# Optimization experiments

Measured on AMD Instinct MI355X. Metric: run time of the kernel, lower is better.

## Reference

```python
import jax, jax.numpy as jnp
import numpy as np

S, P, C = 64, 2048, 32   # num_scenes, num_pixels, scene_channels
A, D, E = 2048, 128, 64  # agent_size, dynamics_features, embed_dim


def setup_inputs() -> dict:
    key = jax.random.key(0)
    ks = jax.random.split(key, 9)
    inv = lambda n: 1.0 / np.sqrt(n)
    return {
        "global_scene": jax.random.normal(ks[0], (S, P, C), jnp.float32),
        "scene_idx": jax.random.randint(ks[1], (A,), 0, S),
        "dynamic_encoding": jax.random.normal(ks[2], (A, D), jnp.float32),
        "W_sn": jax.random.uniform(ks[3], (C, E), jnp.float32, -inv(C), inv(C)),
        "b_sn": jax.random.uniform(ks[4], (E,), jnp.float32, -inv(C), inv(C)),
        "W_df": jax.random.uniform(ks[5], (D, E), jnp.float32, -inv(D), inv(D)),
        "b_df": jax.random.uniform(ks[6], (E,), jnp.float32, -inv(D), inv(D)),
        "w_fc": jax.random.uniform(ks[7], (E,), jnp.float32, -inv(E), inv(E)),
        "b_fc": jax.random.uniform(ks[8], (1,), jnp.float32, -inv(E), inv(E)),
    }


def reference(global_scene, scene_idx, dynamic_encoding, W_sn, b_sn, W_df, b_df, w_fc, b_fc):
    # att1: [S, P, E]; att2: [A, E]
    att1 = jnp.einsum('spc,ce->spe', global_scene, W_sn) + b_sn
    att2 = dynamic_encoding @ W_df + b_df
    # gather scenes per agent, fuse add + relu: [A, P, E]
    add_fusion = jax.nn.relu(att1[scene_idx] + att2[:, None, :])
    # linear to scalar score per pixel, softmax over pixels (dim=1)
    logits = jnp.einsum('ape,e->ap', add_fusion, w_fc) + b_fc[0]  # [A, P]
    alpha = jax.nn.softmax(logits, axis=1)[:, :, None]            # [A, P, 1]
    # alpha-weighted pooling of gathered scene features -> [A, C]
    return jnp.sum(alpha * global_scene[scene_idx], axis=1)
```

## Files before the change

### kernel.cpp

```cpp
#include <hip/hip_runtime.h>
#include <hip/hip_bf16.h>

#define S_ 64
#define P_ 2048
#define C_ 32
#define A_ 2048
#define D_ 128
#define E_ 64

#define LPX   128
#define NLCH  (P_ / LPX)

__global__ __launch_bounds__(256) void att2s_kernel(
    const float* __restrict__ de, const float* __restrict__ Wdf,
    const float* __restrict__ bdf, const int* __restrict__ sidx,
    float* __restrict__ att2, int* __restrict__ counts,
    int* __restrict__ lists, float* __restrict__ Z) {
  __shared__ float4 Wl[128 * 16];
  __shared__ float4 bl[16];
  __shared__ float  dl[16 * 128];
  const int tid = threadIdx.x;

  if (blockIdx.x == 0 && tid < A_ / 4)
    ((float4*)Z)[tid] = make_float4(0.f, 0.f, 0.f, 0.f);

  if (tid < 16) {
    const int a = blockIdx.x * 16 + tid;
    const int s = sidx[a];
    const int pos = atomicAdd(&counts[s], 1);
    lists[s * A_ + pos] = a;
  }

  const float4* W4 = (const float4*)Wdf;
#pragma unroll
  for (int i = 0; i < 8; ++i) Wl[tid + i * 256] = W4[tid + i * 256];
  if (tid < 16) bl[tid] = ((const float4*)bdf)[tid];
  const long base = (long)blockIdx.x * (16 * 128);
#pragma unroll
  for (int i = 0; i < 8; ++i) dl[tid + i * 256] = de[base + tid + i * 256];
  __syncthreads();

  const int r = tid >> 4, e4 = tid & 15;
  float4 acc = bl[e4];
#pragma unroll 4
  for (int d = 0; d < 128; ++d) {
    const float  g = dl[r * 128 + d];
    const float4 w = Wl[d * 16 + e4];
    acc.x = fmaf(g, w.x, acc.x);
    acc.y = fmaf(g, w.y, acc.y);
    acc.z = fmaf(g, w.z, acc.z);
    acc.w = fmaf(g, w.w, acc.w);
  }
  ((float4*)att2)[((long)blockIdx.x * 16 + r) * 16 + e4] = acc;
}

__global__ __launch_bounds__(256) void fused_kernel(
    const float* __restrict__ gs, const float* __restrict__ Wsn,
    const float* __restrict__ bsn, const float* __restrict__ wfc,
    const float* __restrict__ att2, const int* __restrict__ counts,
    const int* __restrict__ lists, float* __restrict__ partial,
    float* __restrict__ Z) {
  const int s   = blockIdx.x >> 4;
  const int ch  = blockIdx.x & (NLCH - 1);
  const int p0  = ch * LPX;
  const int tid = threadIdx.x;
  const int px  = tid >> 1;
  const int eh  = tid & 1;

  __shared__ float  gsl[LPX][36];
  __shared__ float  ubuf[32 * 132];
  __shared__ float4 a2l[32][16];
  __shared__ int    aidl[32];

  float4* Wl4 = (float4*)ubuf;
  float (*alpha_l)[132] = (float(*)[132])ubuf;

  const float4* W4 = (const float4*)Wsn;
  Wl4[tid]       = W4[tid];
  Wl4[tid + 256] = W4[tid + 256];

  const float4* g4 = (const float4*)(gs + ((long)s * P_ + p0) * C_);
#pragma unroll
  for (int k = 0; k < 4; ++k) {
    const int f = tid + k * 256;
    const float4 v = g4[f];
    const int pp = f >> 3, c0 = (f & 7) * 4;
    gsl[pp][c0]     = v.x;
    gsl[pp][c0 + 1] = v.y;
    gsl[pp][c0 + 2] = v.z;
    gsl[pp][c0 + 3] = v.w;
  }

  const float4* wf4 = (const float4*)wfc;
  const float4* b4  = (const float4*)bsn;
  float4 wf[8], a1[8];
#pragma unroll
  for (int q = 0; q < 8; ++q) { wf[q] = wf4[eh * 8 + q]; a1[q] = b4[eh * 8 + q]; }
  __syncthreads();

#pragma unroll
  for (int c = 0; c < 32; ++c) {
    const float g = gsl[px][c];
#pragma unroll
    for (int q = 0; q < 8; ++q) {
      const float4 w = Wl4[c * 16 + eh * 8 + q];
      a1[q].x = fmaf(g, w.x, a1[q].x);
      a1[q].y = fmaf(g, w.y, a1[q].y);
      a1[q].z = fmaf(g, w.z, a1[q].z);
      a1[q].w = fmaf(g, w.w, a1[q].w);
    }
  }

  const int j2 = tid >> 3;
  const int c4 = tid & 7;
  const int n_s = counts[s];

  for (int g0 = 0; g0 < n_s; g0 += 32) {
    const int m = min(32, n_s - g0);
    __syncthreads();
#pragma unroll
    for (int k = 0; k < 2; ++k) {
      const int idx = tid + k * 256;
      const int j = idx >> 4, e4 = idx & 15;
      if (j < m) {
        const int aj = lists[s * A_ + g0 + j];
        a2l[j][e4] = ((const float4*)att2)[aj * 16 + e4];
        if (e4 == 0) aidl[j] = aj;
      }
    }
    __syncthreads();

    for (int j = 0; j < m; ++j) {
      float c0 = 0.f, c1 = 0.f, c2 = 0.f, c3 = 0.f;
#pragma unroll
      for (int q = 0; q < 8; ++q) {
        const float4 t = a2l[j][eh * 8 + q];
        const float4 w = wf[q];
        const float4 av = a1[q];
        c0 = fmaf(fmaxf(av.x + t.x, 0.f), w.x, c0);
        c1 = fmaf(fmaxf(av.y + t.y, 0.f), w.y, c1);
        c2 = fmaf(fmaxf(av.z + t.z, 0.f), w.z, c2);
        c3 = fmaf(fmaxf(av.w + t.w, 0.f), w.w, c3);
      }
      float r = (c0 + c1) + (c2 + c3);
      r += __shfl_xor(r, 1);
      if (eh == 0) alpha_l[j][px] = __expf(r);
    }
    __syncthreads();

    if (j2 < m) {
      const int a = aidl[j2];
      float4 a0 = make_float4(0.f, 0.f, 0.f, 0.f);
      float4 a1p = make_float4(0.f, 0.f, 0.f, 0.f);
      float4 a2p = make_float4(0.f, 0.f, 0.f, 0.f);
      float4 a3p = make_float4(0.f, 0.f, 0.f, 0.f);
      float  zs = 0.f;
#pragma unroll 4
      for (int p4 = 0; p4 < LPX / 4; ++p4) {
        const float w0 = alpha_l[j2][p4 * 4 + 0];
        const float w1 = alpha_l[j2][p4 * 4 + 1];
        const float w2 = alpha_l[j2][p4 * 4 + 2];
        const float w3 = alpha_l[j2][p4 * 4 + 3];
        const float4 v0 = *(const float4*)&gsl[p4 * 4 + 0][c4 * 4];
        const float4 v1 = *(const float4*)&gsl[p4 * 4 + 1][c4 * 4];
        const float4 v2 = *(const float4*)&gsl[p4 * 4 + 2][c4 * 4];
        const float4 v3 = *(const float4*)&gsl[p4 * 4 + 3][c4 * 4];
        zs += (w0 + w1) + (w2 + w3);
        a0.x = fmaf(w0, v0.x, a0.x); a0.y = fmaf(w0, v0.y, a0.y);
        a0.z = fmaf(w0, v0.z, a0.z); a0.w = fmaf(w0, v0.w, a0.w);
        a1p.x = fmaf(w1, v1.x, a1p.x); a1p.y = fmaf(w1, v1.y, a1p.y);
        a1p.z = fmaf(w1, v1.z, a1p.z); a1p.w = fmaf(w1, v1.w, a1p.w);
        a2p.x = fmaf(w2, v2.x, a2p.x); a2p.y = fmaf(w2, v2.y, a2p.y);
        a2p.z = fmaf(w2, v2.z, a2p.z); a2p.w = fmaf(w2, v2.w, a2p.w);
        a3p.x = fmaf(w3, v3.x, a3p.x); a3p.y = fmaf(w3, v3.y, a3p.y);
        a3p.z = fmaf(w3, v3.z, a3p.z); a3p.w = fmaf(w3, v3.w, a3p.w);
      }
      const float4 acc = make_float4((a0.x + a1p.x) + (a2p.x + a3p.x),
                                     (a0.y + a1p.y) + (a2p.y + a3p.y),
                                     (a0.z + a1p.z) + (a2p.z + a3p.z),
                                     (a0.w + a1p.w) + (a2p.w + a3p.w));
      *(float4*)(partial + (long)ch * (A_ * C_) + (long)a * C_ + c4 * 4) = acc;
      if (c4 == 0) atomicAdd(&Z[a], zs);
    }
  }
}

__global__ __launch_bounds__(256) void norm_kernel(
    const float* __restrict__ partial, const float* __restrict__ Z,
    float* __restrict__ out) {
  const int i = blockIdx.x * 256 + threadIdx.x;
  float sum = 0.f;
#pragma unroll
  for (int ch = 0; ch < NLCH; ++ch) sum += partial[(long)ch * (A_ * C_) + i];
  out[i] = sum / Z[i >> 5];
}

extern "C" void kernel_launch(void* const* d_in, const int* in_sizes, int n_in,
                              void* d_out, int out_size, void* d_ws, size_t ws_size,
                              hipStream_t stream) {
  const float* gs   = (const float*)d_in[0];
  const int*   sidx = (const int*)  d_in[1];
  const float* de   = (const float*)d_in[2];
  const float* Wsn  = (const float*)d_in[3];
  const float* bsn  = (const float*)d_in[4];
  const float* Wdf  = (const float*)d_in[5];
  const float* bdf  = (const float*)d_in[6];
  const float* wfc  = (const float*)d_in[7];
  float* out = (float*)d_out;

  float* att2    = (float*)d_ws;
  float* Z       = att2 + (long)A_ * E_;
  int*   counts  = (int*)(Z + A_);
  int*   lists   = counts + 64;
  float* partial = (float*)(lists + (long)S_ * A_);

  hipMemsetAsync(counts, 0, 64 * sizeof(int), stream);
  att2s_kernel<<<A_ / 16,   256, 0, stream>>>(de, Wdf, bdf, sidx, att2,
                                              counts, lists, Z);
  fused_kernel<<<S_ * NLCH, 256, 0, stream>>>(gs, Wsn, bsn, wfc, att2,
                                              counts, lists, partial, Z);
  norm_kernel <<<(A_ * C_) / 256, 256, 0, stream>>>(partial, Z, out);
}
```

Baseline: 141.7 us.

## Fuse normalization into main kernel via last-block reduction and drop memset

Folds the final partial-sum normalization into the fused kernel: each chunk block bumps a per-scene counter, and the last block for a scene reduces the 16 partials and divides by Z. Scene list building moves to a single block doing a deterministic scan, which removes the memset launch and the global atomics. The agent group size drops from 32 to 16, and pooling now uses float2 per thread so all 256 threads stay busy. In exchange, block 0 of the prep kernel runs a serial 2048-iteration scan per scene, the tail reduction runs on only 64 blocks, and the added group iterations bring more barriers.

Result: slower. 288.9 us (+103.9%).

```diff
diff --git a/kernel.cpp b/kernel.cpp
--- a/kernel.cpp
+++ b/kernel.cpp
@@ -1,5 +1,4 @@
 #include <hip/hip_runtime.h>
-#include <hip/hip_bf16.h>
 
 #define S_ 64
 #define P_ 2048
@@ -8,27 +7,32 @@
 #define D_ 128
 #define E_ 64
 
-#define LPX   128
-#define NLCH  (P_ / LPX)
-
-__global__ __launch_bounds__(256) void att2s_kernel(
+#define LPX  128
+#define NLCH (P_ / LPX)
+#define GRP  16
+
+__global__ __launch_bounds__(256) void prep_kernel(
     const float* __restrict__ de, const float* __restrict__ Wdf,
     const float* __restrict__ bdf, const int* __restrict__ sidx,
     float* __restrict__ att2, int* __restrict__ counts,
-    int* __restrict__ lists, float* __restrict__ Z) {
+    int* __restrict__ lists, float* __restrict__ Z,
+    int* __restrict__ scene_done) {
   __shared__ float4 Wl[128 * 16];
   __shared__ float4 bl[16];
   __shared__ float  dl[16 * 128];
+  __shared__ int    sl[A_];
   const int tid = threadIdx.x;
 
-  if (blockIdx.x == 0 && tid < A_ / 4)
-    ((float4*)Z)[tid] = make_float4(0.f, 0.f, 0.f, 0.f);
-
-  if (tid < 16) {
-    const int a = blockIdx.x * 16 + tid;
-    const int s = sidx[a];
-    const int pos = atomicAdd(&counts[s], 1);
-    lists[s * A_ + pos] = a;
+  if (blockIdx.x == 0) {
+    for (int i = tid; i < A_; i += 256) { Z[i] = 0.f; sl[i] = sidx[i]; }
+    if (tid < S_) scene_done[tid] = 0;
+    __syncthreads();
+    if (tid < S_) {
+      int cnt = 0;
+      for (int a = 0; a < A_; ++a)
+        if (sl[a] == tid) lists[tid * A_ + cnt++] = a;
+      counts[tid] = cnt;
+    }
   }
 
   const float4* W4 = (const float4*)Wdf;
@@ -59,7 +63,8 @@
     const float* __restrict__ bsn, const float* __restrict__ wfc,
     const float* __restrict__ att2, const int* __restrict__ counts,
     const int* __restrict__ lists, float* __restrict__ partial,
-    float* __restrict__ Z) {
+    float* __restrict__ Z, int* __restrict__ scene_done,
+    float* __restrict__ out) {
   const int s   = blockIdx.x >> 4;
   const int ch  = blockIdx.x & (NLCH - 1);
   const int p0  = ch * LPX;
@@ -68,9 +73,10 @@
   const int eh  = tid & 1;
 
   __shared__ float  gsl[LPX][36];
-  __shared__ float  ubuf[32 * 132];
-  __shared__ float4 a2l[32][16];
-  __shared__ int    aidl[32];
+  __shared__ float  ubuf[GRP * 132];
+  __shared__ float4 a2l[GRP][16];
+  __shared__ int    aidl[GRP];
+  __shared__ int    lastFlag;
 
   float4* Wl4 = (float4*)ubuf;
   float (*alpha_l)[132] = (float(*)[132])ubuf;
@@ -111,17 +117,15 @@
     }
   }
 
-  const int j2 = tid >> 3;
-  const int c4 = tid & 7;
+  const int j2 = tid >> 4;
+  const int cp = tid & 15;
   const int n_s = counts[s];
 
-  for (int g0 = 0; g0 < n_s; g0 += 32) {
-    const int m = min(32, n_s - g0);
-    __syncthreads();
-#pragma unroll
-    for (int k = 0; k < 2; ++k) {
-      const int idx = tid + k * 256;
-      const int j = idx >> 4, e4 = idx & 15;
+  for (int g0 = 0; g0 < n_s; g0 += GRP) {
+    const int m = min(GRP, n_s - g0);
+    __syncthreads();
+    {
+      const int j = tid >> 4, e4 = tid & 15;
       if (j < m) {
         const int aj = lists[s * A_ + g0 + j];
         a2l[j][e4] = ((const float4*)att2)[aj * 16 + e4];
@@ -150,49 +154,51 @@
 
     if (j2 < m) {
       const int a = aidl[j2];
-      float4 a0 = make_float4(0.f, 0.f, 0.f, 0.f);
-      float4 a1p = make_float4(0.f, 0.f, 0.f, 0.f);
-      float4 a2p = make_float4(0.f, 0.f, 0.f, 0.f);
-      float4 a3p = make_float4(0.f, 0.f, 0.f, 0.f);
+      float2 s0 = make_float2(0.f, 0.f), s1 = make_float2(0.f, 0.f);
+      float2 s2 = make_float2(0.f, 0.f), s3 = make_float2(0.f, 0.f);
       float  zs = 0.f;
 #pragma unroll 4
-      for (int p4 = 0; p4 < LPX / 4; ++p4) {
-        const float w0 = alpha_l[j2][p4 * 4 + 0];
-        const float w1 = alpha_l[j2][p4 * 4 + 1];
-        const float w2 = alpha_l[j2][p4 * 4 + 2];
-        const float w3 = alpha_l[j2][p4 * 4 + 3];
-        const float4 v0 = *(const float4*)&gsl[p4 * 4 + 0][c4 * 4];
-        const float4 v1 = *(const float4*)&gsl[p4 * 4 + 1][c4 * 4];
-        const float4 v2 = *(const float4*)&gsl[p4 * 4 + 2][c4 * 4];
-        const float4 v3 = *(const float4*)&gsl[p4 * 4 + 3][c4 * 4];
+      for (int p = 0; p < LPX; p += 4) {
+        const float w0 = alpha_l[j2][p + 0];
+        const float w1 = alpha_l[j2][p + 1];
+        const float w2 = alpha_l[j2][p + 2];
+        const float w3 = alpha_l[j2][p + 3];
+        const float2 v0 = *(const float2*)&gsl[p + 0][cp * 2];
+        const float2 v1 = *(const float2*)&gsl[p + 1][cp * 2];
+        const float2 v2 = *(const float2*)&gsl[p + 2][cp * 2];
+        const float2 v3 = *(const float2*)&gsl[p + 3][cp * 2];
         zs += (w0 + w1) + (w2 + w3);
-        a0.x = fmaf(w0, v0.x, a0.x); a0.y = fmaf(w0, v0.y, a0.y);
-        a0.z = fmaf(w0, v0.z, a0.z); a0.w = fmaf(w0, v0.w, a0.w);
-        a1p.x = fmaf(w1, v1.x, a1p.x); a1p.y = fmaf(w1, v1.y, a1p.y);
-        a1p.z = fmaf(w1, v1.z, a1p.z); a1p.w = fmaf(w1, v1.w, a1p.w);
-        a2p.x = fmaf(w2, v2.x, a2p.x); a2p.y = fmaf(w2, v2.y, a2p.y);
-        a2p.z = fmaf(w2, v2.z, a2p.z); a2p.w = fmaf(w2, v2.w, a2p.w);
-        a3p.x = fmaf(w3, v3.x, a3p.x); a3p.y = fmaf(w3, v3.y, a3p.y);
-        a3p.z = fmaf(w3, v3.z, a3p.z); a3p.w = fmaf(w3, v3.w, a3p.w);
+        s0.x = fmaf(w0, v0.x, s0.x); s0.y = fmaf(w0, v0.y, s0.y);
+        s1.x = fmaf(w1, v1.x, s1.x); s1.y = fmaf(w1, v1.y, s1.y);
+        s2.x = fmaf(w2, v2.x, s2.x); s2.y = fmaf(w2, v2.y, s2.y);
+        s3.x = fmaf(w3, v3.x, s3.x); s3.y = fmaf(w3, v3.y, s3.y);
       }
-      const float4 acc = make_float4((a0.x + a1p.x) + (a2p.x + a3p.x),
-                                     (a0.y + a1p.y) + (a2p.y + a3p.y),
-                                     (a0.z + a1p.z) + (a2p.z + a3p.z),
-                                     (a0.w + a1p.w) + (a2p.w + a3p.w));
-      *(float4*)(partial + (long)ch * (A_ * C_) + (long)a * C_ + c4 * 4) = acc;
-      if (c4 == 0) atomicAdd(&Z[a], zs);
-    }
-  }
-}
-
-__global__ __launch_bounds__(256) void norm_kernel(
-    const float* __restrict__ partial, const float* __restrict__ Z,
-    float* __restrict__ out) {
-  const int i = blockIdx.x * 256 + threadIdx.x;
-  float sum = 0.f;
-#pragma unroll
-  for (int ch = 0; ch < NLCH; ++ch) sum += partial[(long)ch * (A_ * C_) + i];
-  out[i] = sum / Z[i >> 5];
+      const float2 acc = make_float2((s0.x + s1.x) + (s2.x + s3.x),
+                                     (s0.y + s1.y) + (s2.y + s3.y));
+      *(float2*)(partial + (long)ch * (A_ * C_) + (long)a * C_ + cp * 2) = acc;
+      if (cp == 0) atomicAdd(&Z[a], zs);
+    }
+  }
+
+  __syncthreads();
+  if (tid == 0) {
+    __threadfence();
+    lastFlag = (atomicAdd(&scene_done[s], 1) == NLCH - 1);
+  }
+  __syncthreads();
+  if (lastFlag) {
+    __threadfence();
+    for (int i = tid; i < n_s * C_; i += 256) {
+      const int j = i >> 5;
+      const int c = i & 31;
+      const int a = lists[s * A_ + j];
+      float sum = 0.f;
+#pragma unroll
+      for (int cc = 0; cc < NLCH; ++cc)
+        sum += partial[(long)cc * (A_ * C_) + (long)a * C_ + c];
+      out[(long)a * C_ + c] = sum / Z[a];
+    }
+  }
 }
 
 extern "C" void kernel_launch(void* const* d_in, const int* in_sizes, int n_in,
@@ -208,16 +214,16 @@
   const float* wfc  = (const float*)d_in[7];
   float* out = (float*)d_out;
 
-  float* att2    = (float*)d_ws;
-  float* Z       = att2 + (long)A_ * E_;
-  int*   counts  = (int*)(Z + A_);
-  int*   lists   = counts + 64;
-  float* partial = (float*)(lists + (long)S_ * A_);
-
-  hipMemsetAsync(counts, 0, 64 * sizeof(int), stream);
-  att2s_kernel<<<A_ / 16,   256, 0, stream>>>(de, Wdf, bdf, sidx, att2,
-                                              counts, lists, Z);
+  float* att2       = (float*)d_ws;
+  float* Z          = att2 + (long)A_ * E_;
+  int*   counts     = (int*)(Z + A_);
+  int*   scene_done = counts + 64;
+  int*   lists      = scene_done + 64;
+  float* partial    = (float*)(lists + (long)S_ * A_);
+
+  prep_kernel <<<A_ / 16,   256, 0, stream>>>(de, Wdf, bdf, sidx, att2,
+                                              counts, lists, Z, scene_done);
   fused_kernel<<<S_ * NLCH, 256, 0, stream>>>(gs, Wsn, bsn, wfc, att2,
-                                              counts, lists, partial, Z);
-  norm_kernel <<<(A_ * C_) / 256, 256, 0, stream>>>(partial, Z, out);
+                                              counts, lists, partial, Z,
+                                              scene_done, out);
 }
```

## Widen fused kernel to 256-pixel chunks with 512 threads and per-channel pooling

Applied to the files above, without the earlier changes.

Each fused block now covers 256 pixels with 512 threads, which halves the number of pixel chunks. That in turn halves the partial buffer traffic and the per-block overhead of loading W_sn and the per-agent att2 tiles. Agents are processed in groups of 16 instead of 32. The pooling stage maps one thread per output channel doing scalar FMAs instead of float4 vectors, and the shared-memory padding changes to 34. In exchange, the larger blocks may lower occupancy, and fewer blocks are spread across the CUs.

After: 138.5 us. 1.02x faster.

```diff
diff --git a/kernel.cpp b/kernel.cpp
--- a/kernel.cpp
+++ b/kernel.cpp
@@ -1,5 +1,4 @@
 #include <hip/hip_runtime.h>
-#include <hip/hip_bf16.h>
 
 #define S_ 64
 #define P_ 2048
@@ -8,10 +7,12 @@
 #define D_ 128
 #define E_ 64
 
-#define LPX   128
-#define NLCH  (P_ / LPX)
-
-__global__ __launch_bounds__(256) void att2s_kernel(
+#define LPX  256
+#define NLCH (P_ / LPX)
+#define GRP  16
+#define THR  512
+
+__global__ __launch_bounds__(256) void prep_kernel(
     const float* __restrict__ de, const float* __restrict__ Wdf,
     const float* __restrict__ bdf, const int* __restrict__ sidx,
     float* __restrict__ att2, int* __restrict__ counts,
@@ -21,9 +22,9 @@
   __shared__ float  dl[16 * 128];
   const int tid = threadIdx.x;
 
-  if (blockIdx.x == 0 && tid < A_ / 4)
-    ((float4*)Z)[tid] = make_float4(0.f, 0.f, 0.f, 0.f);
-
+  if (blockIdx.x == 0) {
+    for (int i = tid; i < A_; i += 256) Z[i] = 0.f;
+  }
   if (tid < 16) {
     const int a = blockIdx.x * 16 + tid;
     const int s = sidx[a];
@@ -54,35 +55,33 @@
   ((float4*)att2)[((long)blockIdx.x * 16 + r) * 16 + e4] = acc;
 }
 
-__global__ __launch_bounds__(256) void fused_kernel(
+__global__ __launch_bounds__(THR) void fused_kernel(
     const float* __restrict__ gs, const float* __restrict__ Wsn,
     const float* __restrict__ bsn, const float* __restrict__ wfc,
     const float* __restrict__ att2, const int* __restrict__ counts,
     const int* __restrict__ lists, float* __restrict__ partial,
     float* __restrict__ Z) {
-  const int s   = blockIdx.x >> 4;
+  const int s   = blockIdx.x >> 3;
   const int ch  = blockIdx.x & (NLCH - 1);
   const int p0  = ch * LPX;
   const int tid = threadIdx.x;
   const int px  = tid >> 1;
   const int eh  = tid & 1;
 
-  __shared__ float  gsl[LPX][36];
-  __shared__ float  ubuf[32 * 132];
-  __shared__ float4 a2l[32][16];
-  __shared__ int    aidl[32];
+  __shared__ float  gsl[LPX][34];
+  __shared__ float  ubuf[GRP * 260];
+  __shared__ float4 a2l[GRP][16];
+  __shared__ int    aidl[GRP];
 
   float4* Wl4 = (float4*)ubuf;
-  float (*alpha_l)[132] = (float(*)[132])ubuf;
-
-  const float4* W4 = (const float4*)Wsn;
-  Wl4[tid]       = W4[tid];
-  Wl4[tid + 256] = W4[tid + 256];
+  float (*alpha_l)[260] = (float(*)[260])ubuf;
+
+  Wl4[tid] = ((const float4*)Wsn)[tid];
 
   const float4* g4 = (const float4*)(gs + ((long)s * P_ + p0) * C_);
 #pragma unroll
   for (int k = 0; k < 4; ++k) {
-    const int f = tid + k * 256;
+    const int f = tid + k * THR;
     const float4 v = g4[f];
     const int pp = f >> 3, c0 = (f & 7) * 4;
     gsl[pp][c0]     = v.x;
@@ -111,17 +110,15 @@
     }
   }
 
-  const int j2 = tid >> 3;
-  const int c4 = tid & 7;
+  const int j2 = tid >> 5;
+  const int c2 = tid & 31;
   const int n_s = counts[s];
 
-  for (int g0 = 0; g0 < n_s; g0 += 32) {
-    const int m = min(32, n_s - g0);
+  for (int g0 = 0; g0 < n_s; g0 += GRP) {
+    const int m = min(GRP, n_s - g0);
     __syncthreads();
-#pragma unroll
-    for (int k = 0; k < 2; ++k) {
-      const int idx = tid + k * 256;
-      const int j = idx >> 4, e4 = idx & 15;
+    if (tid < GRP * 16) {
+      const int j = tid >> 4, e4 = tid & 15;
       if (j < m) {
         const int aj = lists[s * A_ + g0 + j];
         a2l[j][e4] = ((const float4*)att2)[aj * 16 + e4];
@@ -131,18 +128,18 @@
     __syncthreads();
 
     for (int j = 0; j < m; ++j) {
-      float c0 = 0.f, c1 = 0.f, c2 = 0.f, c3 = 0.f;
+      float c0 = 0.f, c1 = 0.f, c2s = 0.f, c3 = 0.f;
 #pragma unroll
       for (int q = 0; q < 8; ++q) {
         const float4 t = a2l[j][eh * 8 + q];
         const float4 w = wf[q];
         const float4 av = a1[q];
-        c0 = fmaf(fmaxf(av.x + t.x, 0.f), w.x, c0);
-        c1 = fmaf(fmaxf(av.y + t.y, 0.f), w.y, c1);
-        c2 = fmaf(fmaxf(av.z + t.z, 0.f), w.z, c2);
-        c3 = fmaf(fmaxf(av.w + t.w, 0.f), w.w, c3);
+        c0  = fmaf(fmaxf(av.x + t.x, 0.f), w.x, c0);
+        c1  = fmaf(fmaxf(av.y + t.y, 0.f), w.y, c1);
+        c2s = fmaf(fmaxf(av.z + t.z, 0.f), w.z, c2s);
+        c3  = fmaf(fmaxf(av.w + t.w, 0.f), w.w, c3);
       }
-      float r = (c0 + c1) + (c2 + c3);
+      float r = (c0 + c1) + (c2s + c3);
       r += __shfl_xor(r, 1);
       if (eh == 0) alpha_l[j][px] = __expf(r);
     }
@@ -150,37 +147,23 @@
 
     if (j2 < m) {
       const int a = aidl[j2];
-      float4 a0 = make_float4(0.f, 0.f, 0.f, 0.f);
-      float4 a1p = make_float4(0.f, 0.f, 0.f, 0.f);
-      float4 a2p = make_float4(0.f, 0.f, 0.f, 0.f);
-      float4 a3p = make_float4(0.f, 0.f, 0.f, 0.f);
-      float  zs = 0.f;
-#pragma unroll 4
-      for (int p4 = 0; p4 < LPX / 4; ++p4) {
-        const float w0 = alpha_l[j2][p4 * 4 + 0];
-        const float w1 = alpha_l[j2][p4 * 4 + 1];
-        const float w2 = alpha_l[j2][p4 * 4 + 2];
-        const float w3 = alpha_l[j2][p4 * 4 + 3];
-        const float4 v0 = *(const float4*)&gsl[p4 * 4 + 0][c4 * 4];
-        const float4 v1 = *(const float4*)&gsl[p4 * 4 + 1][c4 * 4];
-        const float4 v2 = *(const float4*)&gsl[p4 * 4 + 2][c4 * 4];
-        const float4 v3 = *(const float4*)&gsl[p4 * 4 + 3][c4 * 4];
-        zs += (w0 + w1) + (w2 + w3);
-        a0.x = fmaf(w0, v0.x, a0.x); a0.y = fmaf(w0, v0.y, a0.y);
-        a0.z = fmaf(w0, v0.z, a0.z); a0.w = fmaf(w0, v0.w, a0.w);
-        a1p.x = fmaf(w1, v1.x, a1p.x); a1p.y = fmaf(w1, v1.y, a1p.y);
-        a1p.z = fmaf(w1, v1.z, a1p.z); a1p.w = fmaf(w1, v1.w, a1p.w);
-        a2p.x = fmaf(w2, v2.x, a2p.x); a2p.y = fmaf(w2, v2.y, a2p.y);
-        a2p.z = fmaf(w2, v2.z, a2p.z); a2p.w = fmaf(w2, v2.w, a2p.w);
-        a3p.x = fmaf(w3, v3.x, a3p.x); a3p.y = fmaf(w3, v3.y, a3p.y);
-        a3p.z = fmaf(w3, v3.z, a3p.z); a3p.w = fmaf(w3, v3.w, a3p.w);
+      float s0 = 0.f, s1 = 0.f, s2 = 0.f, s3 = 0.f;
+      float z0 = 0.f, z1 = 0.f, z2 = 0.f, z3 = 0.f;
+#pragma unroll 2
+      for (int p = 0; p < LPX; p += 4) {
+        const float w0 = alpha_l[j2][p + 0];
+        const float w1 = alpha_l[j2][p + 1];
+        const float w2 = alpha_l[j2][p + 2];
+        const float w3 = alpha_l[j2][p + 3];
+        s0 = fmaf(w0, gsl[p + 0][c2], s0);
+        s1 = fmaf(w1, gsl[p + 1][c2], s1);
+        s2 = fmaf(w2, gsl[p + 2][c2], s2);
+        s3 = fmaf(w3, gsl[p + 3][c2], s3);
+        z0 += w0; z1 += w1; z2 += w2; z3 += w3;
       }
-      const float4 acc = make_float4((a0.x + a1p.x) + (a2p.x + a3p.x),
-                                     (a0.y + a1p.y) + (a2p.y + a3p.y),
-                                     (a0.z + a1p.z) + (a2p.z + a3p.z),
-                                     (a0.w + a1p.w) + (a2p.w + a3p.w));
-      *(float4*)(partial + (long)ch * (A_ * C_) + (long)a * C_ + c4 * 4) = acc;
-      if (c4 == 0) atomicAdd(&Z[a], zs);
+      partial[(long)ch * (A_ * C_) + (long)a * C_ + c2] =
+          (s0 + s1) + (s2 + s3);
+      if (c2 == 0) atomicAdd(&Z[a], (z0 + z1) + (z2 + z3));
     }
   }
 }
@@ -215,9 +198,9 @@
   float* partial = (float*)(lists + (long)S_ * A_);
 
   hipMemsetAsync(counts, 0, 64 * sizeof(int), stream);
-  att2s_kernel<<<A_ / 16,   256, 0, stream>>>(de, Wdf, bdf, sidx, att2,
+  prep_kernel <<<A_ / 16,   256, 0, stream>>>(de, Wdf, bdf, sidx, att2,
                                               counts, lists, Z);
-  fused_kernel<<<S_ * NLCH, 256, 0, stream>>>(gs, Wsn, bsn, wfc, att2,
+  fused_kernel<<<S_ * NLCH, THR, 0, stream>>>(gs, Wsn, bsn, wfc, att2,
                                               counts, lists, partial, Z);
   norm_kernel <<<(A_ * C_) / 256, 256, 0, stream>>>(partial, Z, out);
 }
```
